# Kernel tuning notes

Measured on AMD Instinct MI355X. Metric: run time of the kernel, lower is better.

Reference implementation:

```python
import jax, jax.numpy as jnp
import numpy as np

EMBED = 2048
MLP = 8192
EPS = 1e-5


def setup_inputs() -> dict:
    key = jax.random.key(0)
    ks = jax.random.split(key, 16)
    s = 0.02
    inp = {
        "x": jax.random.normal(ks[0], (2, 2048, EMBED), dtype=jnp.float32),
        "wq": jax.random.normal(ks[1], (EMBED, EMBED), dtype=jnp.float32) * s,
        "bq": jnp.zeros((EMBED,), jnp.float32),
        "wk": jax.random.normal(ks[2], (EMBED, EMBED), dtype=jnp.float32) * s,
        "bk": jnp.zeros((EMBED,), jnp.float32),
        "wv": jax.random.normal(ks[3], (EMBED, EMBED), dtype=jnp.float32) * s,
        "bv": jnp.zeros((EMBED,), jnp.float32),
        "wd": jax.random.normal(ks[4], (EMBED, EMBED), dtype=jnp.float32) * s,
        "bd": jnp.zeros((EMBED,), jnp.float32),
        "ln_g": jnp.ones((EMBED,), jnp.float32),
        "ln_b": jnp.zeros((EMBED,), jnp.float32),
        "w1": jax.random.normal(ks[5], (MLP, EMBED), dtype=jnp.float32) * s,
        "b1": jnp.zeros((MLP,), jnp.float32),
        "w2": jax.random.normal(ks[6], (EMBED, MLP), dtype=jnp.float32) * s,
        "b2": jnp.zeros((EMBED,), jnp.float32),
    }
    return inp


def _layernorm(x, g, b):
    mu = jnp.mean(x, axis=-1, keepdims=True)
    var = jnp.mean(jnp.square(x - mu), axis=-1, keepdims=True)
    return (x - mu) * jax.lax.rsqrt(var + EPS) * g + b


def reference(x, wq, bq, wk, bk, wv, bv, wd, bd, ln_g, ln_b, w1, b1, w2, b2):
    # Single-head attention; scale uses full embed_dim (rotary_emb.dim == embed_dim).
    q = jnp.einsum("bse,fe->bsf", x, wq) + bq
    k = jnp.einsum("bse,fe->bsf", x, wk) + bk
    v = jnp.einsum("bse,fe->bsf", x, wv) + bv
    scores = jnp.einsum("bqe,bke->bqk", q, k) / jnp.sqrt(jnp.float32(EMBED))
    probs = jax.nn.softmax(scores, axis=-1)
    ctx = jnp.einsum("bqk,bke->bqe", probs, v)
    attn_out = jnp.einsum("bse,fe->bsf", ctx, wd) + bd
    # residual (dropout is identity in eval mode)
    h = x + attn_out
    h = _layernorm(h, ln_g, ln_b)
    mlp = jnp.einsum("bse,fe->bsf", h, w1) + b1
    mlp = jax.nn.gelu(mlp, approximate=False)
    mlp = jnp.einsum("bsf,ef->bse", mlp, w2) + b2
    return h + mlp
```

## Files before the change

### kernel.cpp

```cpp
#include <hip/hip_runtime.h>
#include <math.h>


#define SEQ 2048
#define EMB 2048
#define MLPD 8192

typedef __attribute__((ext_vector_type(8))) short short8;
typedef __attribute__((ext_vector_type(4))) float floatx4;
typedef unsigned short ushort;

__device__ __forceinline__ short f2bf(float f) {
  union { float f; unsigned u; } v; v.f = f;
  unsigned r = v.u + 0x7FFFu + ((v.u >> 16) & 1u);
  return (short)(r >> 16);
}

__device__ __forceinline__ void gload16(const ushort* g, ushort* l) {
  __builtin_amdgcn_global_load_lds(
      (__attribute__((address_space(1))) void*)g,
      (__attribute__((address_space(3))) void*)(unsigned)(unsigned long)l,
      16, 0, 0);
}

enum { EPI_QKV = 0, EPI_SCORES = 1, EPI_PV = 2, EPI_RES = 3, EPI_GELU = 4 };

template<int EPI>
__global__ __launch_bounds__(512, 2)
void gemm256(const ushort* __restrict__ A, const ushort* __restrict__ B,
             const float* __restrict__ bias, void* __restrict__ Cp,
             int N, int K, int lda, int ldb, int ldc,
             long sA, long sB, long sC, float scale)
{
  extern __shared__ ushort lds[];
  const int t = threadIdx.x;
  const int lane = t & 63, w = t >> 6;
  const int wm = w >> 2, wn = w & 3;
  const long bm = (long)blockIdx.y * 256;
  const long bn = (long)blockIdx.x * 256;
  A += (long)blockIdx.z * sA;
  B += (long)blockIdx.z * sB;

  const int srow = (w << 3) + (lane >> 3);
  const int gcol = (lane & 7) ^ ((lane >> 3) & 7);
  const ushort* Ab = A + (bm + srow) * (long)lda + gcol * 8;
  const ushort* Bb = B + (bn + srow) * (long)ldb + gcol * 8;
  ushort* lw = lds + (w << 9);

#define STG_A0(LOFF, KK) do { gload16(Ab + (KK), lw + (LOFF)); \
    gload16(Ab + 64L * lda + (KK), lw + (LOFF) + 4096); } while (0)
#define STG_A1(LOFF, KK) do { gload16(Ab + 128L * lda + (KK), lw + (LOFF)); \
    gload16(Ab + 192L * lda + (KK), lw + (LOFF) + 4096); } while (0)
#define STG_B0(LOFF, KK) do { gload16(Bb + (KK), lw + (LOFF)); \
    gload16(Bb + 64L * ldb + (KK), lw + (LOFF) + 4096); } while (0)
#define STG_B1(LOFF, KK) do { gload16(Bb + 128L * ldb + (KK), lw + (LOFF)); \
    gload16(Bb + 192L * ldb + (KK), lw + (LOFF) + 4096); } while (0)

  const int l15 = lane & 15, q = lane >> 4, swz = l15 & 7;
  const int kx0 = (q ^ swz) << 3;
  const int kx1 = ((4 + q) ^ swz) << 3;
  const int arow = (wm << 13) + l15 * 64;
  const int brow = 16384 + ((wn >> 1) << 13) + ((wn & 1) << 12) + l15 * 64;

  floatx4 acc[8][4];
#pragma unroll
  for (int m = 0; m < 8; ++m)
#pragma unroll
    for (int n = 0; n < 4; ++n) acc[m][n] = (floatx4)0.0f;

  short8 A0[4], A1[4], B0[4], B1[4];

#define LDS8(IDX) (*(const short8*)&lds[IDX])
#define RD_ALK0(CB) do { _Pragma("unroll") for (int mf = 0; mf < 4; ++mf) \
    A0[mf] = LDS8((CB) + arow + mf * 1024 + kx0); } while (0)
#define RD_ALK1(CB) do { _Pragma("unroll") for (int mf = 0; mf < 4; ++mf) \
    A1[mf] = LDS8((CB) + arow + mf * 1024 + kx1); } while (0)
#define RD_AHK0(CB) do { _Pragma("unroll") for (int mf = 0; mf < 4; ++mf) \
    A0[mf] = LDS8((CB) + arow + (4 + mf) * 1024 + kx0); } while (0)
#define RD_AHK1(CB) do { _Pragma("unroll") for (int mf = 0; mf < 4; ++mf) \
    A1[mf] = LDS8((CB) + arow + (4 + mf) * 1024 + kx1); } while (0)
#define RD_BK0(CB) do { _Pragma("unroll") for (int nf = 0; nf < 4; ++nf) \
    B0[nf] = LDS8((CB) + brow + nf * 1024 + kx0); } while (0)
#define RD_BK1(CB) do { _Pragma("unroll") for (int nf = 0; nf < 4; ++nf) \
    B1[nf] = LDS8((CB) + brow + nf * 1024 + kx1); } while (0)

#define MMA16(MO, AX, BX) do {                                            \
    __builtin_amdgcn_s_setprio(1);                                        \
    _Pragma("unroll") for (int mf = 0; mf < 4; ++mf)                      \
      _Pragma("unroll") for (int nf = 0; nf < 4; ++nf)                    \
        acc[(MO)+mf][nf] = __builtin_amdgcn_mfma_f32_16x16x32_bf16(       \
            AX[mf], BX[nf], acc[(MO)+mf][nf], 0, 0, 0);                   \
    __builtin_amdgcn_s_setprio(0);                                        \
  } while (0)

#define BARR() __builtin_amdgcn_s_barrier()
#define VMC4  asm volatile("s_waitcnt vmcnt(4)" ::: "memory")

#define KTILE(CB, NB, K1, K2) do {                                        \
     RD_ALK0(CB); RD_BK0(CB); STG_A0((NB) + 0, K1);              \
              MMA16(0, A0, B0); BARR();                                   \
     RD_ALK1(CB); RD_BK1(CB); STG_A1((NB) + 8192, K1);           \
              MMA16(0, A1, B1); BARR();                                   \
     RD_AHK0(CB); STG_B0((CB) + 16384, K2);                      \
              MMA16(4, A0, B0); BARR();                                   \
     RD_AHK1(CB); STG_B1((CB) + 24576, K2);                      \
              MMA16(4, A1, B1); VMC4; BARR();                             \
  } while (0)

  STG_A0(0, 0);              STG_A1(8192, 0);
  STG_B0(16384, 0);          STG_B1(24576, 0);
  {
    const int k1p = (K > 64) ? 64 : 0;
    STG_B0(32768 + 16384, k1p);
    STG_B1(32768 + 24576, k1p);
  }
  asm volatile("s_waitcnt vmcnt(4)" ::: "memory");
  BARR();

  const int NT = K >> 6;
  for (int kt = 0; kt < NT; kt += 2) {
    const int k1 = ((kt + 1 < NT) ? kt + 1 : NT - 1) << 6;
    const int k2 = ((kt + 2 < NT) ? kt + 2 : NT - 1) << 6;
    const int k3 = ((kt + 3 < NT) ? kt + 3 : NT - 1) << 6;
    KTILE(0,     32768, k1, k2);
    KTILE(32768, 0,     k2, k3);
  }
  asm volatile("s_waitcnt vmcnt(0)" ::: "memory");
#undef KTILE
#undef MMA16
#undef RD_ALK0
#undef RD_ALK1
#undef RD_AHK0
#undef RD_AHK1
#undef RD_BK0
#undef RD_BK1
#undef LDS8
#undef STG_A0
#undef STG_A1
#undef STG_B0
#undef STG_B1

  const int lq = lane >> 4;
#pragma unroll
  for (int mf = 0; mf < 8; ++mf) {
#pragma unroll
    for (int nf = 0; nf < 4; ++nf) {
#pragma unroll
      for (int i = 0; i < 4; ++i) {
        const long r = bm + wm * 128 + mf * 16 + lq * 4 + i;
        const long c = bn + wn * 64 + nf * 16 + l15;
        float val = acc[mf][nf][i];
        if constexpr (EPI == EPI_QKV) {
          val += bias[c];
          ((ushort*)Cp)[r * (long)ldc + c] = (ushort)f2bf(val);
        } else if constexpr (EPI == EPI_SCORES) {
          ((float*)Cp)[(long)blockIdx.z * sC + r * (long)ldc + c] = val * scale;
        } else {
          val += bias[c];
          float g = 0.5f * val * (1.0f + erff(val * 0.70710678118f));
          ((ushort*)Cp)[r * (long)ldc + c] = (ushort)f2bf(g);
        }
      }
    }
  }
}

template<int EPI>
__global__ __launch_bounds__(256)
void gemm_bt(const ushort* __restrict__ A, const ushort* __restrict__ B,
             const float* __restrict__ bias, const float* __restrict__ res,
             void* __restrict__ Cp, int N, int K,
             int lda, int ldb, int ldc,
             long sA, long sB, long sC, float scale)
{
  __shared__ ushort As[128 * 32];
  __shared__ ushort Bs[128 * 32];

  const int t = threadIdx.x;
  const int lane = t & 63, wid = t >> 6;
  const int wm = wid >> 1, wn = wid & 1;
  const long bm = (long)blockIdx.y * 128;
  const long bn = (long)blockIdx.x * 128;
  A += (long)blockIdx.z * sA;
  B += (long)blockIdx.z * sB;

  const int srow = (wid << 5) + (lane >> 2);
  const int scol = (lane & 3) << 3;
  const ushort* a0 = A + (bm + srow) * (long)lda + scol;
  const ushort* a1 = a0 + 16L * lda;
  const ushort* b0 = B + (bn + srow) * (long)ldb + scol;
  const ushort* b1 = b0 + 16L * ldb;
  ushort* lA0 = As + (wid << 10);
  ushort* lA1 = lA0 + 512;
  ushort* lB0 = Bs + (wid << 10);
  ushort* lB1 = lB0 + 512;

  floatx4 acc[4][4];
#pragma unroll
  for (int m = 0; m < 4; ++m)
#pragma unroll
    for (int n = 0; n < 4; ++n) acc[m][n] = (floatx4)0.0f;

  const int l15 = lane & 15, kq = (lane >> 4) << 3;
  const int abase = ((wm << 6) + l15) * 32 + kq;
  const int bbase = ((wn << 6) + l15) * 32 + kq;

  for (int kb = 0; kb < K; kb += 32) {
    gload16(a0 + kb, lA0);
    gload16(a1 + kb, lA1);
    gload16(b0 + kb, lB0);
    gload16(b1 + kb, lB1);
    __syncthreads();

    short8 a[4], b[4];
#pragma unroll
    for (int m = 0; m < 4; ++m)
      a[m] = *reinterpret_cast<const short8*>(&As[abase + m * (16 * 32)]);
#pragma unroll
    for (int n = 0; n < 4; ++n)
      b[n] = *reinterpret_cast<const short8*>(&Bs[bbase + n * (16 * 32)]);
#pragma unroll
    for (int m = 0; m < 4; ++m)
#pragma unroll
      for (int n = 0; n < 4; ++n)
        acc[m][n] = __builtin_amdgcn_mfma_f32_16x16x32_bf16(a[m], b[n], acc[m][n], 0, 0, 0);
    __syncthreads();
  }

  const int lq = lane >> 4;
#pragma unroll
  for (int m = 0; m < 4; ++m) {
#pragma unroll
    for (int n = 0; n < 4; ++n) {
#pragma unroll
      for (int i = 0; i < 4; ++i) {
        const long r = bm + wm * 64 + m * 16 + lq * 4 + i;
        const long c = bn + wn * 64 + n * 16 + l15;
        float val = acc[m][n][i];
        if constexpr (EPI == EPI_SCORES) {
          ((float*)Cp)[(long)blockIdx.z * sC + r * (long)ldc + c] = val * scale;
        } else if constexpr (EPI == EPI_PV) {
          ((ushort*)Cp)[(long)blockIdx.z * sC + r * (long)ldc + c] = (ushort)f2bf(val);
        }
      }
    }
  }
}

__global__ __launch_bounds__(256)
void reduce2(const float* __restrict__ p0, const float* __restrict__ p1,
             const float* __restrict__ bias, const float* __restrict__ res,
             float* __restrict__ out)
{
  const long i = ((long)blockIdx.x * 256 + threadIdx.x) * 8;
  const int c = (int)(i & 2047);
  float4 a0 = *(const float4*)(p0 + i),  a1 = *(const float4*)(p0 + i + 4);
  float4 q0 = *(const float4*)(p1 + i),  q1 = *(const float4*)(p1 + i + 4);
  float4 r0 = *(const float4*)(res + i), r1 = *(const float4*)(res + i + 4);
  float4 b0 = *(const float4*)(bias + c), b1 = *(const float4*)(bias + c + 4);
  float4 o0 = {a0.x + q0.x + r0.x + b0.x, a0.y + q0.y + r0.y + b0.y,
               a0.z + q0.z + r0.z + b0.z, a0.w + q0.w + r0.w + b0.w};
  float4 o1 = {a1.x + q1.x + r1.x + b1.x, a1.y + q1.y + r1.y + b1.y,
               a1.z + q1.z + r1.z + b1.z, a1.w + q1.w + r1.w + b1.w};
  *(float4*)(out + i) = o0;
  *(float4*)(out + i + 4) = o1;
}

__global__ __launch_bounds__(256)
void cvt8(const float* __restrict__ s, ushort* __restrict__ d) {
  const long i = ((long)blockIdx.x * 256 + threadIdx.x) * 8;
  float4 a = *reinterpret_cast<const float4*>(s + i);
  float4 b = *reinterpret_cast<const float4*>(s + i + 4);
  short8 v;
  v[0] = f2bf(a.x); v[1] = f2bf(a.y); v[2] = f2bf(a.z); v[3] = f2bf(a.w);
  v[4] = f2bf(b.x); v[5] = f2bf(b.y); v[6] = f2bf(b.z); v[7] = f2bf(b.w);
  *reinterpret_cast<short8*>(d + i) = v;
}

__global__ __launch_bounds__(256)
void concat3(const float* __restrict__ b0, const float* __restrict__ b1,
             const float* __restrict__ b2, float* __restrict__ dst) {
  const int i = blockIdx.x * 256 + threadIdx.x;
  dst[i] = (i < 2048) ? b0[i] : (i < 4096) ? b1[i - 2048] : b2[i - 4096];
}

__global__ __launch_bounds__(256)
void transpose_v(const ushort* __restrict__ qkv, ushort* __restrict__ vT) {
  __shared__ ushort tile[32][33];
  const int b = blockIdx.z;
  const int s0 = blockIdx.x * 32, e0 = blockIdx.y * 32;
  const int tx = threadIdx.x & 31, ty = threadIdx.x >> 5;
#pragma unroll
  for (int i = 0; i < 4; ++i) {
    const long s = (long)b * SEQ + s0 + ty + i * 8;
    tile[ty + i * 8][tx] = qkv[s * 6144 + 4096 + e0 + tx];
  }
  __syncthreads();
#pragma unroll
  for (int i = 0; i < 4; ++i) {
    const long e = (long)b * SEQ + e0 + ty + i * 8;
    vT[e * SEQ + s0 + tx] = tile[tx][ty + i * 8];
  }
}

__global__ __launch_bounds__(256)
void softmax_rows(const float* __restrict__ S, ushort* __restrict__ P) {
  const long row = blockIdx.x;
  const float* src = S + row * 2048;
  const int t = threadIdx.x, lane = t & 63, wid = t >> 6;
  float4 a = *reinterpret_cast<const float4*>(src + t * 8);
  float4 b = *reinterpret_cast<const float4*>(src + t * 8 + 4);
  float v[8] = {a.x, a.y, a.z, a.w, b.x, b.y, b.z, b.w};
  float m = v[0];
#pragma unroll
  for (int i = 1; i < 8; ++i) m = fmaxf(m, v[i]);
#pragma unroll
  for (int o = 32; o; o >>= 1) m = fmaxf(m, __shfl_xor(m, o));
  __shared__ float rm[4], rs[4];
  if (!lane) rm[wid] = m;
  __syncthreads();
  m = fmaxf(fmaxf(rm[0], rm[1]), fmaxf(rm[2], rm[3]));
  float e[8], s = 0.f;
#pragma unroll
  for (int i = 0; i < 8; ++i) { e[i] = __expf(v[i] - m); s += e[i]; }
#pragma unroll
  for (int o = 32; o; o >>= 1) s += __shfl_xor(s, o);
  if (!lane) rs[wid] = s;
  __syncthreads();
  s = rs[0] + rs[1] + rs[2] + rs[3];
  const float inv = 1.0f / s;
  short8 wv;
#pragma unroll
  for (int i = 0; i < 8; ++i) wv[i] = f2bf(e[i] * inv);
  *reinterpret_cast<short8*>(P + row * 2048 + t * 8) = wv;
}

__global__ __launch_bounds__(256)
void layernorm_fused(const float* __restrict__ p0, const float* __restrict__ p1,
                     const float* __restrict__ bias, const float* __restrict__ res,
                     const float* __restrict__ g, const float* __restrict__ bb,
                     float* __restrict__ H, ushort* __restrict__ Hb) {
  const long row = blockIdx.x;
  const long base = row * 2048;
  const int t = threadIdx.x, lane = t & 63, wid = t >> 6;
  const long i = base + t * 8;
  const int c0 = t * 8;
  float v[8];
  {
    float4 a0 = *(const float4*)(p0 + i),  a1 = *(const float4*)(p0 + i + 4);
    float4 q0 = *(const float4*)(p1 + i),  q1 = *(const float4*)(p1 + i + 4);
    float4 r0 = *(const float4*)(res + i), r1 = *(const float4*)(res + i + 4);
    float4 b0 = *(const float4*)(bias + c0), b1 = *(const float4*)(bias + c0 + 4);
    v[0] = a0.x + q0.x + r0.x + b0.x; v[1] = a0.y + q0.y + r0.y + b0.y;
    v[2] = a0.z + q0.z + r0.z + b0.z; v[3] = a0.w + q0.w + r0.w + b0.w;
    v[4] = a1.x + q1.x + r1.x + b1.x; v[5] = a1.y + q1.y + r1.y + b1.y;
    v[6] = a1.z + q1.z + r1.z + b1.z; v[7] = a1.w + q1.w + r1.w + b1.w;
  }
  float s = 0.f, ss = 0.f;
#pragma unroll
  for (int i2 = 0; i2 < 8; ++i2) { s += v[i2]; ss += v[i2] * v[i2]; }
#pragma unroll
  for (int o = 32; o; o >>= 1) { s += __shfl_xor(s, o); ss += __shfl_xor(ss, o); }
  __shared__ float r1s[4], r2s[4];
  if (!lane) { r1s[wid] = s; r2s[wid] = ss; }
  __syncthreads();
  s = r1s[0] + r1s[1] + r1s[2] + r1s[3];
  ss = r2s[0] + r2s[1] + r2s[2] + r2s[3];
  const float mu = s * (1.0f / 2048.0f);
  const float var = ss * (1.0f / 2048.0f) - mu * mu;
  const float inv = rsqrtf(var + 1e-5f);
  float o0[8];
  short8 wv;
#pragma unroll
  for (int i2 = 0; i2 < 8; ++i2) {
    const int c = c0 + i2;
    o0[i2] = (v[i2] - mu) * inv * g[c] + bb[c];
    wv[i2] = f2bf(o0[i2]);
  }
  float4 w0 = {o0[0], o0[1], o0[2], o0[3]}, w1 = {o0[4], o0[5], o0[6], o0[7]};
  *reinterpret_cast<float4*>(H + i) = w0;
  *reinterpret_cast<float4*>(H + i + 4) = w1;
  *reinterpret_cast<short8*>(Hb + i) = wv;
}

extern "C" void kernel_launch(void* const* d_in, const int* in_sizes, int n_in,
                              void* d_out, int out_size, void* d_ws, size_t ws_size,
                              hipStream_t stream) {
  const float* x    = (const float*)d_in[0];
  const float* wq   = (const float*)d_in[1];
  const float* bq   = (const float*)d_in[2];
  const float* wk   = (const float*)d_in[3];
  const float* bk   = (const float*)d_in[4];
  const float* wv   = (const float*)d_in[5];
  const float* bv   = (const float*)d_in[6];
  const float* wd   = (const float*)d_in[7];
  const float* bd   = (const float*)d_in[8];
  const float* ln_g = (const float*)d_in[9];
  const float* ln_b = (const float*)d_in[10];
  const float* w1   = (const float*)d_in[11];
  const float* b1   = (const float*)d_in[12];
  const float* w2   = (const float*)d_in[13];
  const float* b2   = (const float*)d_in[14];
  float* out = (float*)d_out;

  (void)hipFuncSetAttribute((const void*)&gemm256<EPI_QKV>,
      hipFuncAttributeMaxDynamicSharedMemorySize, 131072);
  (void)hipFuncSetAttribute((const void*)&gemm256<EPI_GELU>,
      hipFuncAttributeMaxDynamicSharedMemorySize, 131072);
  (void)hipFuncSetAttribute((const void*)&gemm256<EPI_SCORES>,
      hipFuncAttributeMaxDynamicSharedMemorySize, 131072);

  char* p = (char*)d_ws;
  const size_t MB = 1048576;
  ushort* wdb    = (ushort*)(p + 0 * MB);
  ushort* w1b    = (ushort*)(p + 8 * MB);
  ushort* w2b    = (ushort*)(p + 40 * MB);
  float*  bqkv   = (float*) (p + 72 * MB);
  ushort* xb     = (ushort*)(p + 73 * MB);
  ushort* probs  = xb;
  ushort* qkv    = (ushort*)(p + 89 * MB);
  float*  partA  = (float*) (p + 89 * MB);
  ushort* mlpb   = (ushort*)(p + 89 * MB);
  ushort* vT     = (ushort*)(p + 137 * MB);
  ushort* wqkvb  = (ushort*)(p + 153 * MB);
  float*  scores = (float*) (p + 153 * MB);
  ushort* ctx    = (ushort*)(p + 153 * MB);
  float*  partM0 = (float*) (p + 0 * MB);
  float*  partM1 = (float*) (p + 153 * MB);
  float*  h      = (float*) (p + 185 * MB);
  ushort* hb     = (ushort*)(p + 217 * MB);

  const dim3 blk(256), blk512(512);
  const long SQ = (long)SEQ * SEQ;

  cvt8<<<4096, blk, 0, stream>>>(x, xb);
  cvt8<<<2048, blk, 0, stream>>>(wq, wqkvb);
  cvt8<<<2048, blk, 0, stream>>>(wk, wqkvb + 4194304);
  cvt8<<<2048, blk, 0, stream>>>(wv, wqkvb + 8388608);
  cvt8<<<2048, blk, 0, stream>>>(wd, wdb);
  cvt8<<<8192, blk, 0, stream>>>(w1, w1b);
  cvt8<<<8192, blk, 0, stream>>>(w2, w2b);
  concat3<<<24, blk, 0, stream>>>(bq, bk, bv, bqkv);

  gemm256<EPI_QKV><<<dim3(24, 16, 1), blk512, 131072, stream>>>(
      xb, wqkvb, bqkv, qkv, 6144, 2048, 2048, 2048, 6144, 0, 0, 0, 1.f);

  transpose_v<<<dim3(64, 64, 2), blk, 0, stream>>>(qkv, vT);

  gemm_bt<EPI_SCORES><<<dim3(16, 16, 2), blk, 0, stream>>>(
      qkv, qkv + 2048, nullptr, nullptr, scores, 2048, 2048, 6144, 6144, 2048,
      2048L * 6144, 2048L * 6144, SQ, 0.022097086912079608f);

  softmax_rows<<<dim3(4096), blk, 0, stream>>>(scores, probs);

  gemm_bt<EPI_PV><<<dim3(16, 16, 2), blk, 0, stream>>>(
      probs, vT, nullptr, nullptr, ctx, 2048, 2048, 2048, 2048, 2048,
      SQ, SQ, SQ, 1.f);

  gemm256<EPI_SCORES><<<dim3(8, 16, 2), blk512, 131072, stream>>>(
      ctx, wdb, nullptr, partA, 2048, 1024, 2048, 2048, 2048,
      1024, 1024, 8388608, 1.f);

  layernorm_fused<<<4096, blk, 0, stream>>>(
      partA, partA + 8388608, bd, x, ln_g, ln_b, h, hb);

  gemm256<EPI_GELU><<<dim3(32, 16, 1), blk512, 131072, stream>>>(
      hb, w1b, b1, mlpb, 8192, 2048, 2048, 2048, 8192, 0, 0, 0, 1.f);

  gemm256<EPI_SCORES><<<dim3(8, 16, 2), blk512, 131072, stream>>>(
      mlpb, w2b, nullptr, partM0, 2048, 4096, 8192, 8192, 2048,
      4096, 4096, (long)(153 * MB / 4), 1.f);
  reduce2<<<4096, blk, 0, stream>>>(partM0, partM1, b2, h, out);
}
```

Before: 660.9 us.

## Restructure GEMM main loop into two-phase full-tile double-buffered pipeline

```diff
diff --git a/kernel.cpp b/kernel.cpp
--- a/kernel.cpp
+++ b/kernel.cpp
@@ -68,72 +68,61 @@
 #pragma unroll
     for (int n = 0; n < 4; ++n) acc[m][n] = (floatx4)0.0f;
 
-  short8 A0[4], A1[4], B0[4], B1[4];
+  short8 A0[8], A1[8], B0[4], B1[4];
 
 #define LDS8(IDX) (*(const short8*)&lds[IDX])
-#define RD_ALK0(CB) do { _Pragma("unroll") for (int mf = 0; mf < 4; ++mf) \
-    A0[mf] = LDS8((CB) + arow + mf * 1024 + kx0); } while (0)
-#define RD_ALK1(CB) do { _Pragma("unroll") for (int mf = 0; mf < 4; ++mf) \
-    A1[mf] = LDS8((CB) + arow + mf * 1024 + kx1); } while (0)
-#define RD_AHK0(CB) do { _Pragma("unroll") for (int mf = 0; mf < 4; ++mf) \
-    A0[mf] = LDS8((CB) + arow + (4 + mf) * 1024 + kx0); } while (0)
-#define RD_AHK1(CB) do { _Pragma("unroll") for (int mf = 0; mf < 4; ++mf) \
-    A1[mf] = LDS8((CB) + arow + (4 + mf) * 1024 + kx1); } while (0)
-#define RD_BK0(CB) do { _Pragma("unroll") for (int nf = 0; nf < 4; ++nf) \
-    B0[nf] = LDS8((CB) + brow + nf * 1024 + kx0); } while (0)
-#define RD_BK1(CB) do { _Pragma("unroll") for (int nf = 0; nf < 4; ++nf) \
-    B1[nf] = LDS8((CB) + brow + nf * 1024 + kx1); } while (0)
-
-#define MMA16(MO, AX, BX) do {                                            \
+#define BARR() __builtin_amdgcn_s_barrier()
+
+#define KTILE(CB, KS) do {                                                \
+                                                        \
+    _Pragma("unroll") for (int mf = 0; mf < 8; ++mf)                      \
+      A0[mf] = LDS8((CB) + arow + mf * 1024 + kx0);                       \
+    _Pragma("unroll") for (int nf = 0; nf < 4; ++nf)                      \
+      B0[nf] = LDS8((CB) + brow + nf * 1024 + kx0);                       \
+    _Pragma("unroll") for (int mf = 0; mf < 8; ++mf)                      \
+      A1[mf] = LDS8((CB) + arow + mf * 1024 + kx1);                       \
     __builtin_amdgcn_s_setprio(1);                                        \
-    _Pragma("unroll") for (int mf = 0; mf < 4; ++mf)                      \
+    _Pragma("unroll") for (int mf = 0; mf < 8; ++mf)                      \
       _Pragma("unroll") for (int nf = 0; nf < 4; ++nf)                    \
-        acc[(MO)+mf][nf] = __builtin_amdgcn_mfma_f32_16x16x32_bf16(       \
-            AX[mf], BX[nf], acc[(MO)+mf][nf], 0, 0, 0);                   \
+        acc[mf][nf] = __builtin_amdgcn_mfma_f32_16x16x32_bf16(            \
+            A0[mf], B0[nf], acc[mf][nf], 0, 0, 0);                        \
     __builtin_amdgcn_s_setprio(0);                                        \
-  } while (0)
-
-#define BARR() __builtin_amdgcn_s_barrier()
-#define VMC4  asm volatile("s_waitcnt vmcnt(4)" ::: "memory")
-
-#define KTILE(CB, NB, K1, K2) do {                                        \
-     RD_ALK0(CB); RD_BK0(CB); STG_A0((NB) + 0, K1);              \
-              MMA16(0, A0, B0); BARR();                                   \
-     RD_ALK1(CB); RD_BK1(CB); STG_A1((NB) + 8192, K1);           \
-              MMA16(0, A1, B1); BARR();                                   \
-     RD_AHK0(CB); STG_B0((CB) + 16384, K2);                      \
-              MMA16(4, A0, B0); BARR();                                   \
-     RD_AHK1(CB); STG_B1((CB) + 24576, K2);                      \
-              MMA16(4, A1, B1); VMC4; BARR();                             \
+    _Pragma("unroll") for (int nf = 0; nf < 4; ++nf)                      \
+      B1[nf] = LDS8((CB) + brow + nf * 1024 + kx1);                       \
+    asm volatile("s_waitcnt lgkmcnt(0)" ::: "memory");                    \
+    BARR();                                                               \
+    \
+    STG_A0((CB) + 0, KS);     STG_A1((CB) + 8192, KS);                    \
+    STG_B0((CB) + 16384, KS); STG_B1((CB) + 24576, KS);                   \
+    __builtin_amdgcn_s_setprio(1);                                        \
+    _Pragma("unroll") for (int mf = 0; mf < 8; ++mf)                      \
+      _Pragma("unroll") for (int nf = 0; nf < 4; ++nf)                    \
+        acc[mf][nf] = __builtin_amdgcn_mfma_f32_16x16x32_bf16(            \
+            A1[mf], B1[nf], acc[mf][nf], 0, 0, 0);                        \
+    __builtin_amdgcn_s_setprio(0);                                        \
+    asm volatile("s_waitcnt vmcnt(8)" ::: "memory");                      \
+    BARR();                                                               \
   } while (0)
 
   STG_A0(0, 0);              STG_A1(8192, 0);
   STG_B0(16384, 0);          STG_B1(24576, 0);
   {
     const int k1p = (K > 64) ? 64 : 0;
-    STG_B0(32768 + 16384, k1p);
-    STG_B1(32768 + 24576, k1p);
-  }
-  asm volatile("s_waitcnt vmcnt(4)" ::: "memory");
+    STG_A0(32768 + 0, k1p);     STG_A1(32768 + 8192, k1p);
+    STG_B0(32768 + 16384, k1p); STG_B1(32768 + 24576, k1p);
+  }
+  asm volatile("s_waitcnt vmcnt(8)" ::: "memory");
   BARR();
 
   const int NT = K >> 6;
   for (int kt = 0; kt < NT; kt += 2) {
-    const int k1 = ((kt + 1 < NT) ? kt + 1 : NT - 1) << 6;
     const int k2 = ((kt + 2 < NT) ? kt + 2 : NT - 1) << 6;
     const int k3 = ((kt + 3 < NT) ? kt + 3 : NT - 1) << 6;
-    KTILE(0,     32768, k1, k2);
-    KTILE(32768, 0,     k2, k3);
+    KTILE(0,     k2);
+    KTILE(32768, k3);
   }
   asm volatile("s_waitcnt vmcnt(0)" ::: "memory");
 #undef KTILE
-#undef MMA16
-#undef RD_ALK0
-#undef RD_ALK1
-#undef RD_AHK0
-#undef RD_AHK1
-#undef RD_BK0
-#undef RD_BK1
 #undef LDS8
 #undef STG_A0
 #undef STG_A1
```

New measurement: 676.8 us. +2.4%, slower.

## Compute V transposed directly via GEMM and store attention scores as bf16

Applied to the files above, without the earlier changes.

```diff
diff --git a/kernel.cpp b/kernel.cpp
--- a/kernel.cpp
+++ b/kernel.cpp
@@ -14,6 +14,10 @@
   union { float f; unsigned u; } v; v.f = f;
   unsigned r = v.u + 0x7FFFu + ((v.u >> 16) & 1u);
   return (short)(r >> 16);
+}
+__device__ __forceinline__ float bf2f(ushort u) {
+  union { unsigned u; float f; } v; v.u = ((unsigned)u) << 16;
+  return v.f;
 }
 
 __device__ __forceinline__ void gload16(const ushort* g, ushort* l) {
@@ -23,7 +27,8 @@
       16, 0, 0);
 }
 
-enum { EPI_QKV = 0, EPI_SCORES = 1, EPI_PV = 2, EPI_RES = 3, EPI_GELU = 4 };
+enum { EPI_QKV = 0, EPI_SCORES = 1, EPI_PV = 2, EPI_GELU = 4,
+       EPI_VT = 5, EPI_SBF16 = 6 };
 
 template<int EPI>
 __global__ __launch_bounds__(512, 2)
@@ -97,14 +102,14 @@
 #define VMC4  asm volatile("s_waitcnt vmcnt(4)" ::: "memory")
 
 #define KTILE(CB, NB, K1, K2) do {                                        \
-     RD_ALK0(CB); RD_BK0(CB); STG_A0((NB) + 0, K1);              \
-              MMA16(0, A0, B0); BARR();                                   \
-     RD_ALK1(CB); RD_BK1(CB); STG_A1((NB) + 8192, K1);           \
-              MMA16(0, A1, B1); BARR();                                   \
-     RD_AHK0(CB); STG_B0((CB) + 16384, K2);                      \
-              MMA16(4, A0, B0); BARR();                                   \
-     RD_AHK1(CB); STG_B1((CB) + 24576, K2);                      \
-              MMA16(4, A1, B1); VMC4; BARR();                             \
+    RD_ALK0(CB); RD_BK0(CB); STG_A0((NB) + 0, K1);                        \
+    MMA16(0, A0, B0); BARR();                                             \
+    RD_ALK1(CB); RD_BK1(CB); STG_A1((NB) + 8192, K1);                     \
+    MMA16(0, A1, B1); BARR();                                             \
+    RD_AHK0(CB); STG_B0((CB) + 16384, K2);                                \
+    MMA16(4, A0, B0); BARR();                                             \
+    RD_AHK1(CB); STG_B1((CB) + 24576, K2);                                \
+    MMA16(4, A1, B1); VMC4; BARR();                                       \
   } while (0)
 
   STG_A0(0, 0);              STG_A1(8192, 0);
@@ -168,9 +173,8 @@
 template<int EPI>
 __global__ __launch_bounds__(256)
 void gemm_bt(const ushort* __restrict__ A, const ushort* __restrict__ B,
-             const float* __restrict__ bias, const float* __restrict__ res,
-             void* __restrict__ Cp, int N, int K,
-             int lda, int ldb, int ldc,
+             const float* __restrict__ bias, void* __restrict__ Cp,
+             int N, int K, int lda, int ldb, int ldc,
              long sA, long sB, long sC, float scale)
 {
   __shared__ ushort As[128 * 32];
@@ -237,9 +241,13 @@
         const long r = bm + wm * 64 + m * 16 + lq * 4 + i;
         const long c = bn + wn * 64 + n * 16 + l15;
         float val = acc[m][n][i];
-        if constexpr (EPI == EPI_SCORES) {
-          ((float*)Cp)[(long)blockIdx.z * sC + r * (long)ldc + c] = val * scale;
+        if constexpr (EPI == EPI_SBF16) {
+          ((ushort*)Cp)[(long)blockIdx.z * sC + r * (long)ldc + c] =
+              (ushort)f2bf(val * scale);
         } else if constexpr (EPI == EPI_PV) {
+          ((ushort*)Cp)[(long)blockIdx.z * sC + r * (long)ldc + c] = (ushort)f2bf(val);
+        } else if constexpr (EPI == EPI_VT) {
+          val += bias[r];
           ((ushort*)Cp)[(long)blockIdx.z * sC + r * (long)ldc + c] = (ushort)f2bf(val);
         }
       }
@@ -278,39 +286,21 @@
 }
 
 __global__ __launch_bounds__(256)
-void concat3(const float* __restrict__ b0, const float* __restrict__ b1,
-             const float* __restrict__ b2, float* __restrict__ dst) {
+void concat2(const float* __restrict__ b0, const float* __restrict__ b1,
+             float* __restrict__ dst) {
   const int i = blockIdx.x * 256 + threadIdx.x;
-  dst[i] = (i < 2048) ? b0[i] : (i < 4096) ? b1[i - 2048] : b2[i - 4096];
-}
-
-__global__ __launch_bounds__(256)
-void transpose_v(const ushort* __restrict__ qkv, ushort* __restrict__ vT) {
-  __shared__ ushort tile[32][33];
-  const int b = blockIdx.z;
-  const int s0 = blockIdx.x * 32, e0 = blockIdx.y * 32;
-  const int tx = threadIdx.x & 31, ty = threadIdx.x >> 5;
-#pragma unroll
-  for (int i = 0; i < 4; ++i) {
-    const long s = (long)b * SEQ + s0 + ty + i * 8;
-    tile[ty + i * 8][tx] = qkv[s * 6144 + 4096 + e0 + tx];
-  }
-  __syncthreads();
-#pragma unroll
-  for (int i = 0; i < 4; ++i) {
-    const long e = (long)b * SEQ + e0 + ty + i * 8;
-    vT[e * SEQ + s0 + tx] = tile[tx][ty + i * 8];
-  }
-}
-
-__global__ __launch_bounds__(256)
-void softmax_rows(const float* __restrict__ S, ushort* __restrict__ P) {
+  dst[i] = (i < 2048) ? b0[i] : b1[i - 2048];
+}
+
+__global__ __launch_bounds__(256)
+void softmax_rows(const ushort* __restrict__ S, ushort* __restrict__ P) {
   const long row = blockIdx.x;
-  const float* src = S + row * 2048;
+  const ushort* src = S + row * 2048;
   const int t = threadIdx.x, lane = t & 63, wid = t >> 6;
-  float4 a = *reinterpret_cast<const float4*>(src + t * 8);
-  float4 b = *reinterpret_cast<const float4*>(src + t * 8 + 4);
-  float v[8] = {a.x, a.y, a.z, a.w, b.x, b.y, b.z, b.w};
+  short8 raw = *reinterpret_cast<const short8*>(src + t * 8);
+  float v[8];
+#pragma unroll
+  for (int i = 0; i < 8; ++i) v[i] = bf2f((ushort)raw[i]);
   float m = v[0];
 #pragma unroll
   for (int i = 1; i < 8; ++i) m = fmaxf(m, v[i]);
@@ -415,46 +405,49 @@
   ushort* wdb    = (ushort*)(p + 0 * MB);
   ushort* w1b    = (ushort*)(p + 8 * MB);
   ushort* w2b    = (ushort*)(p + 40 * MB);
-  float*  bqkv   = (float*) (p + 72 * MB);
+  float*  bqk    = (float*) (p + 72 * MB);
   ushort* xb     = (ushort*)(p + 73 * MB);
   ushort* probs  = xb;
-  ushort* qkv    = (ushort*)(p + 89 * MB);
+  ushort* qk     = (ushort*)(p + 89 * MB);
+  ushort* wqkb   = (ushort*)(p + 121 * MB);
+  ushort* vT     = (ushort*)(p + 121 * MB);
+  ushort* wvb    = (ushort*)(p + 137 * MB);
+  ushort* scoresb= (ushort*)(p + 137 * MB);
   float*  partA  = (float*) (p + 89 * MB);
   ushort* mlpb   = (ushort*)(p + 89 * MB);
-  ushort* vT     = (ushort*)(p + 137 * MB);
-  ushort* wqkvb  = (ushort*)(p + 153 * MB);
-  float*  scores = (float*) (p + 153 * MB);
-  ushort* ctx    = (ushort*)(p + 153 * MB);
+  float*  h      = (float*) (p + 153 * MB);
+  ushort* hb     = (ushort*)(p + 185 * MB);
+  ushort* ctx    = (ushort*)(p + 201 * MB);
   float*  partM0 = (float*) (p + 0 * MB);
-  float*  partM1 = (float*) (p + 153 * MB);
-  float*  h      = (float*) (p + 185 * MB);
-  ushort* hb     = (ushort*)(p + 217 * MB);
+  float*  partM1 = (float*) (p + 201 * MB);
 
   const dim3 blk(256), blk512(512);
   const long SQ = (long)SEQ * SEQ;
 
   cvt8<<<4096, blk, 0, stream>>>(x, xb);
-  cvt8<<<2048, blk, 0, stream>>>(wq, wqkvb);
-  cvt8<<<2048, blk, 0, stream>>>(wk, wqkvb + 4194304);
-  cvt8<<<2048, blk, 0, stream>>>(wv, wqkvb + 8388608);
+  cvt8<<<2048, blk, 0, stream>>>(wq, wqkb);
+  cvt8<<<2048, blk, 0, stream>>>(wk, wqkb + 4194304);
+  cvt8<<<2048, blk, 0, stream>>>(wv, wvb);
   cvt8<<<2048, blk, 0, stream>>>(wd, wdb);
   cvt8<<<8192, blk, 0, stream>>>(w1, w1b);
   cvt8<<<8192, blk, 0, stream>>>(w2, w2b);
-  concat3<<<24, blk, 0, stream>>>(bq, bk, bv, bqkv);
-
-  gemm256<EPI_QKV><<<dim3(24, 16, 1), blk512, 131072, stream>>>(
-      xb, wqkvb, bqkv, qkv, 6144, 2048, 2048, 2048, 6144, 0, 0, 0, 1.f);
-
-  transpose_v<<<dim3(64, 64, 2), blk, 0, stream>>>(qkv, vT);
-
-  gemm_bt<EPI_SCORES><<<dim3(16, 16, 2), blk, 0, stream>>>(
-      qkv, qkv + 2048, nullptr, nullptr, scores, 2048, 2048, 6144, 6144, 2048,
-      2048L * 6144, 2048L * 6144, SQ, 0.022097086912079608f);
-
-  softmax_rows<<<dim3(4096), blk, 0, stream>>>(scores, probs);
+  concat2<<<16, blk, 0, stream>>>(bq, bk, bqk);
+
+  gemm256<EPI_QKV><<<dim3(16, 16, 1), blk512, 131072, stream>>>(
+      xb, wqkb, bqk, qk, 4096, 2048, 2048, 2048, 4096, 0, 0, 0, 1.f);
+
+  gemm_bt<EPI_VT><<<dim3(16, 16, 2), blk, 0, stream>>>(
+      wvb, xb, bv, vT, 2048, 2048, 2048, 2048, 2048,
+      0, SQ, SQ, 1.f);
+
+  gemm_bt<EPI_SBF16><<<dim3(16, 16, 2), blk, 0, stream>>>(
+      qk, qk + 2048, nullptr, scoresb, 2048, 2048, 4096, 4096, 2048,
+      2048L * 4096, 2048L * 4096, SQ, 0.022097086912079608f);
+
+  softmax_rows<<<dim3(4096), blk, 0, stream>>>(scoresb, probs);
 
   gemm_bt<EPI_PV><<<dim3(16, 16, 2), blk, 0, stream>>>(
-      probs, vT, nullptr, nullptr, ctx, 2048, 2048, 2048, 2048, 2048,
+      probs, vT, nullptr, ctx, 2048, 2048, 2048, 2048, 2048,
       SQ, SQ, SQ, 1.f);
 
   gemm256<EPI_SCORES><<<dim3(8, 16, 2), blk512, 131072, stream>>>(
@@ -469,6 +462,6 @@
 
   gemm256<EPI_SCORES><<<dim3(8, 16, 2), blk512, 131072, stream>>>(
       mlpb, w2b, nullptr, partM0, 2048, 4096, 8192, 8192, 2048,
-      4096, 4096, (long)(153 * MB / 4), 1.f);
+      4096, 4096, (long)(201 * MB / 4), 1.f);
   reduce2<<<4096, blk, 0, stream>>>(partM0, partM1, b2, h, out);
 }
```

Result: no change. 659.3 us (-0.2%).
